# Performance work log

Hardware: AMD Instinct MI355X
Metric: run time of the kernel (lower is better)

Reference implementation:

```python
import jax, jax.numpy as jnp
import numpy as np

B, T, IDIM, HDIM, K, LMAX, NLAYERS = 64, 1024, 120, 320, 72, 96, 3
LAMB = 0.1
NEG = -1e30


def lse3(a, b, c):
    m = jnp.maximum(jnp.maximum(a, b), c)
    return m + jnp.log(jnp.exp(a - m) + jnp.exp(b - m) + jnp.exp(c - m))


def _lstm_dir(x, Wih, Whh, bb):
    # x: [B,T,D] -> h: [B,T,H]; PyTorch gate order i,f,g,o
    gx = jnp.einsum('btd,gd->tbg', x, Wih) + bb  # [T,B,4H]
    def step(carry, g):
        h, c = carry
        g = g + h @ Whh.T
        i, f, gg, o = jnp.split(g, 4, axis=-1)
        c = jax.nn.sigmoid(f) * c + jax.nn.sigmoid(i) * jnp.tanh(gg)
        h = jax.nn.sigmoid(o) * jnp.tanh(c)
        return (h, c), h
    h0 = jnp.zeros((x.shape[0], HDIM), x.dtype)
    _, hs = jax.lax.scan(step, (h0, h0), gx)
    return hs.transpose(1, 0, 2)


def _rev(x, lengths):
    # reverse each sequence within its valid length (packed-sequence semantics)
    t = jnp.arange(x.shape[1])
    idx = jnp.where(t[None, :] < lengths[:, None], lengths[:, None] - 1 - t[None, :], t[None, :])
    return jnp.take_along_axis(x, idx[:, :, None], axis=1)


def _blstm_layer(x, Wih_f, Whh_f, b_f, Wih_b, Whh_b, b_b, lengths):
    hf = _lstm_dir(x, Wih_f, Whh_f, b_f)
    hb = _rev(_lstm_dir(_rev(x, lengths), Wih_b, Whh_b, b_b), lengths)
    return jnp.concatenate([hf, hb], axis=2)


def _ctc_forward(logp, labels, in_lens, lab_lens):
    # standard CTC alpha recursion (blank=0), log-space, vectorized over batch
    Bn, Tn, _ = logp.shape
    S = 2 * LMAX + 1
    ext = jnp.zeros((Bn, S), jnp.int32).at[:, 1::2].set(labels)  # blank-interleaved labels
    em = jnp.take_along_axis(logp, jnp.broadcast_to(ext[:, None, :], (Bn, Tn, S)), axis=2)
    em = em.transpose(1, 0, 2)  # [T,B,S]
    s_idx = jnp.arange(S)
    prev_lab = jnp.concatenate([jnp.full((Bn, 2), -1, jnp.int32), ext[:, :-2]], axis=1)
    can_skip = ((s_idx[None, :] % 2) == 1) & (ext != prev_lab)
    valid_s = s_idx[None, :] < (2 * lab_lens[:, None] + 1)
    alpha0 = jnp.full((Bn, S), NEG, logp.dtype)
    alpha0 = alpha0.at[:, 0].set(em[0][:, 0]).at[:, 1].set(em[0][:, 1])
    alpha0 = jnp.where(valid_s, alpha0, NEG)
    def step(alpha, inp):
        em_t, t = inp
        a2 = jnp.concatenate([jnp.full((Bn, 1), NEG, alpha.dtype), alpha[:, :-1]], axis=1)
        a3 = jnp.concatenate([jnp.full((Bn, 2), NEG, alpha.dtype), alpha[:, :-2]], axis=1)
        a3 = jnp.where(can_skip, a3, NEG)
        new = lse3(alpha, a2, a3) + em_t
        new = jnp.where(valid_s, new, NEG)
        new = jnp.where((t < in_lens)[:, None], new, alpha)  # freeze past utterance end
        return new, None
    alpha, _ = jax.lax.scan(step, alpha0, (em[1:], jnp.arange(1, Tn)))
    last = 2 * lab_lens
    aL = jnp.take_along_axis(alpha, last[:, None], axis=1)[:, 0]
    aLm1 = jnp.take_along_axis(alpha, (last - 1)[:, None], axis=1)[:, 0]
    return jnp.logaddexp(aL, aLm1)  # log p(labels | x)


def setup_inputs():
    key = jax.random.key(0)
    ks = jax.random.split(key, 12)
    H4 = 4 * HDIM
    s = 0.05
    return dict(
        logits=jax.random.normal(ks[0], (B, T, IDIM), jnp.float32),
        labels_padded=jax.random.randint(ks[1], (B, LMAX), 1, K).astype(jnp.int32),
        input_lengths=jax.random.randint(ks[2], (B,), T // 2, T + 1).astype(jnp.int32),
        label_lengths=jax.random.randint(ks[3], (B,), LMAX // 2, LMAX + 1).astype(jnp.int32),
        Wih0=jax.random.normal(ks[4], (2, H4, IDIM), jnp.float32) * s,
        Whh0=jax.random.normal(ks[5], (2, H4, HDIM), jnp.float32) * s,
        b0=jnp.zeros((2, H4), jnp.float32),
        Wih=jax.random.normal(ks[6], (NLAYERS - 1, 2, H4, 2 * HDIM), jnp.float32) * s,
        Whh=jax.random.normal(ks[7], (NLAYERS - 1, 2, H4, HDIM), jnp.float32) * s,
        b=jnp.zeros((NLAYERS - 1, 2, H4), jnp.float32),
        W_lin=jax.random.normal(ks[8], (K, 2 * HDIM), jnp.float32) * s,
        b_lin=jnp.zeros((K,), jnp.float32),
    )


def reference(logits, labels_padded, input_lengths, label_lengths, Wih0, Whh0, b0, Wih, Whh, b, W_lin, b_lin):
    # sort by input length descending (mirrors torch.sort + index_select)
    order = jnp.argsort(-input_lengths)
    logits = logits[order]
    labels_padded = labels_padded[order]
    input_lengths = input_lengths[order]
    label_lengths = label_lengths[order]
    # 3-layer BLSTM encoder
    x = _blstm_layer(logits, Wih0[0], Whh0[0], b0[0], Wih0[1], Whh0[1], b0[1], input_lengths)
    for l in range(NLAYERS - 1):
        x = _blstm_layer(x, Wih[l, 0], Whh[l, 0], b[l, 0], Wih[l, 1], Whh[l, 1], b[l, 1], input_lengths)
    netout = jax.nn.log_softmax(x @ W_lin.T + b_lin, axis=2)  # [B,T,K]
    # CTC-CRF: numerator = CTC alpha log-prob; denominator = free-running partition
    num = _ctc_forward(netout, labels_padded, input_lengths, label_lengths)
    tmask = jnp.arange(netout.shape[1])[None, :] < input_lengths[:, None]
    den = jnp.sum(jnp.where(tmask, jax.nn.logsumexp(netout, axis=2), 0.0), axis=1)
    return jnp.mean(den - (1.0 + LAMB) * num)
```

## Files before the change

### kernel.cpp

```cpp
#include <hip/hip_runtime.h>
#include <cstdint>
#include <cstddef>


typedef _Float16 f16;
typedef _Float16 h2v   __attribute__((ext_vector_type(2)));
typedef _Float16 f16x8 __attribute__((ext_vector_type(8)));
typedef float    f32x4 __attribute__((ext_vector_type(4)));
typedef uint32_t u32x4 __attribute__((ext_vector_type(4)));

#define NEGF (-1e30f)
#define CT 128

__device__ __forceinline__ float dot2f(h2v a, h2v b, float c) {
#if __has_builtin(__builtin_amdgcn_fdot2)
  return __builtin_amdgcn_fdot2(a, b, c, false);
#else
  return c + (float)a.x * (float)b.x + (float)a.y * (float)b.y;
#endif
}

__device__ __forceinline__ void stage16(f16* lds, const f16* g) {
#if __has_builtin(__builtin_amdgcn_global_load_lds)
  __builtin_amdgcn_global_load_lds(
      (const __attribute__((address_space(1))) uint32_t*)g,
      (__attribute__((address_space(3))) uint32_t*)lds, 16, 0, 0);
#else
  int lane = threadIdx.x & 63;
  *(f16x8*)&lds[lane * 8] = *(const f16x8*)g;
#endif
}


__global__ void conv_logits(const float* __restrict__ src, f16* __restrict__ dst) {
  int idx = blockIdx.x * 256 + threadIdx.x;
  int row = idx >> 7, k = idx & 127;
  dst[idx] = (f16)((k < 120) ? src[(size_t)row * 120 + k] : 0.f);
}

__global__ void conv_wt0(const float* __restrict__ w, f16* __restrict__ dst) {
  int idx = blockIdx.x * 256 + threadIdx.x;
  int n = idx >> 7, k = idx & 127;
  dst[idx] = (f16)((k < 120) ? w[(size_t)n * 120 + k] : 0.f);
}

__global__ void conv_copy(const float* __restrict__ src, f16* __restrict__ dst, int count) {
  int idx = blockIdx.x * 256 + threadIdx.x;
  if (idx < count) dst[idx] = (f16)src[idx];
}

__global__ void conv_wtl(const float* __restrict__ w, f16* __restrict__ dst) {
  int idx = blockIdx.x * 256 + threadIdx.x;
  int n = idx / 640, k = idx % 640;
  dst[idx] = (f16)((n < 72) ? w[(size_t)n * 640 + k] : 0.f);
}

__global__ void conv_whh(const float* __restrict__ whh0, const float* __restrict__ whh,
                         uint32_t* __restrict__ dst) {
  int o = blockIdx.x * 256 + threadIdx.x;
  int tid = o & 511;
  int g  = o >> 9;
  int j  = g % 40;
  int g2 = g / 40;
  int i  = g2 % 5;
  int g3 = g2 / 5;
  int hf = g3 & 1, slot = g3 >> 1;
  int tau = i * 512 + tid;
  int lr = tau >> 2, kq = tau & 3;
  int gate = lr / 160, u = lr - gate * 160;
  int r = gate * 320 + hf * 160 + u;
  int k = kq * 80 + j * 2;
  const float* srcm = (slot < 2) ? (whh0 + ((size_t)slot * 1280 + r) * 320)
                                 : (whh  + ((size_t)(slot - 2) * 1280 + r) * 320);
  f16 lo = (f16)srcm[k], hi = (f16)srcm[k + 1];
  dst[o] = (uint32_t)__builtin_bit_cast(unsigned short, lo) |
           ((uint32_t)__builtin_bit_cast(unsigned short, hi) << 16);
}

__global__ __launch_bounds__(256)
void gemm_chunk(const f16* __restrict__ A, const f16* __restrict__ W,
                f16* __restrict__ gxc, const int* __restrict__ lens,
                int lda, int kTiles, int c0) {
  __shared__ __align__(16) f16 As[128 * 32];
  __shared__ __align__(16) f16 Ws[128 * 32];
  const int tid = threadIdx.x;
  const int lane = tid & 63, wid = tid >> 6;
  const int wm = wid >> 1, wn = wid & 1;
  const int dir = blockIdx.y >> 6, b = blockIdx.y & 63;
  const int n0 = blockIdx.x * 128;
  const int r_base = lane >> 2;
  const int c8 = (lane & 3) * 8;
  const int len = lens[b];

  f32x4 acc[4][4] = {};

  for (int kt = 0; kt < kTiles; ++kt) {
    const int k0 = kt * 32;
    __syncthreads();
#pragma unroll
    for (int hh = 0; hh < 2; ++hh) {
      const int c = wid * 2 + hh;
      const int j = c * 16 + r_base;
      const int s = c0 * CT + j;
      const int tt = dir ? ((s < len) ? (len - 1 - s) : s) : s;
      const f16* gA = A + (size_t)(b * 1024 + tt) * lda + k0 + c8;
      const f16* gW = W + (size_t)(dir * 1280 + n0 + c * 16 + r_base) * lda + k0 + c8;
      stage16(&As[c * 512], gA);
      stage16(&Ws[c * 512], gW);
    }
    __syncthreads();

    const int koff = (lane >> 4) * 8;
    f16x8 av[4], wv[4];
#pragma unroll
    for (int i = 0; i < 4; ++i)
      av[i] = *(const f16x8*)&As[(wm * 64 + i * 16 + (lane & 15)) * 32 + koff];
#pragma unroll
    for (int i = 0; i < 4; ++i)
      wv[i] = *(const f16x8*)&Ws[(wn * 64 + i * 16 + (lane & 15)) * 32 + koff];
#pragma unroll
    for (int i = 0; i < 4; ++i)
#pragma unroll
      for (int j = 0; j < 4; ++j)
        acc[i][j] = __builtin_amdgcn_mfma_f32_16x16x32_f16(av[i], wv[j], acc[i][j], 0, 0, 0);
  }

  const int r0 = (lane >> 4) * 4, cn = lane & 15;
  const size_t obase = (size_t)(dir * 64 + b) * CT;
#pragma unroll
  for (int i = 0; i < 4; ++i) {
    const int m = wm * 64 + i * 16 + r0;
#pragma unroll
    for (int j = 0; j < 4; ++j) {
      const int n = n0 + wn * 64 + j * 16 + cn;
#pragma unroll
      for (int r = 0; r < 4; ++r)
        gxc[(obase + m + r) * 1280 + n] = (f16)acc[i][j][r];
    }
  }
}

__global__ void __launch_bounds__(512)
__attribute__((amdgpu_waves_per_eu(2, 2)))
lstm_scan_chunk(const volatile uint32_t* wbuf,
                const f16* __restrict__ gxc,
                const float* __restrict__ bias,
                const int* __restrict__ lens,
                f16* xnext,
                uint32_t* xq,
                f16* hsave,
                float* csave,
                int layer, int c0) {
  const int wg = blockIdx.x;
  const int half = wg >> 7;
  const int bd = wg & 127;
  const int b = bd >> 1, dir = bd & 1;
  const int tid = threadIdx.x;

  __shared__ __align__(16) f16 hbuf[320];
  __shared__ float ylds[640];
  __shared__ __align__(16) f16 hstage[64 * 160];

  h2v w[5][40];
  {
    const volatile uint32_t* wb =
        wbuf + (size_t)((layer * 2 + dir) * 2 + half) * 200 * 512;
#pragma unroll
    for (int i = 0; i < 5; ++i)
#pragma unroll
      for (int j = 0; j < 40; ++j) {
        uint32_t v = wb[(i * 40 + j) * 512 + tid];
        w[i][j] = __builtin_bit_cast(h2v, v);
      }
  }
  if (tid < 320) hbuf[tid] = (c0 == 0) ? (f16)0.f : hsave[bd * 320 + tid];

  const int len = lens[b];
  const int kq = tid & 3;
  const int qi = tid >> 2;
  const int gu = half * 160 + tid;
  float c_state = 0.f;
  float bi = 0.f, bff = 0.f, bg = 0.f, bo = 0.f;
  if (tid < 160) {
    if (c0 > 0) c_state = csave[wg * 160 + tid];
    const float* bp = bias + dir * 1280 + gu;
    bi = bp[0]; bff = bp[320]; bg = bp[640]; bo = bp[960];
  }
  __syncthreads();

  const size_t grow0 = (size_t)(dir * 64 + b) * CT;

  for (int tl = 0; tl < CT; ++tl) {
    const int s = c0 * CT + tl;
    const uint32_t tag = (uint32_t)(layer * 1024 + s + 1);

    float gxi = 0.f, gxf = 0.f, gxg = 0.f, gxo = 0.f;
    if (tid < 160) {
      const f16* gp = gxc + (grow0 + tl) * 1280 + gu;
      gxi = (float)gp[0]; gxf = (float)gp[320]; gxg = (float)gp[640]; gxo = (float)gp[960];
    }

    float a0 = 0.f, a1 = 0.f, a2 = 0.f, a3 = 0.f, a4 = 0.f;
    {
      const u32x4* h4 = (const u32x4*)hbuf;
#pragma unroll
      for (int jb = 0; jb < 5; ++jb) {
        u32x4 p = h4[kq * 10 + jb * 2];
        u32x4 q = h4[kq * 10 + jb * 2 + 1];
        h2v hr[8];
#pragma unroll
        for (int j = 0; j < 4; ++j) hr[j] = __builtin_bit_cast(h2v, p[j]);
#pragma unroll
        for (int j = 0; j < 4; ++j) hr[4 + j] = __builtin_bit_cast(h2v, q[j]);
#pragma unroll
        for (int j = 0; j < 8; ++j) {
          a0 = dot2f(w[0][jb * 8 + j], hr[j], a0);
          a1 = dot2f(w[1][jb * 8 + j], hr[j], a1);
          a2 = dot2f(w[2][jb * 8 + j], hr[j], a2);
          a3 = dot2f(w[3][jb * 8 + j], hr[j], a3);
          a4 = dot2f(w[4][jb * 8 + j], hr[j], a4);
        }
      }
    }
    {
      float av[5] = {a0, a1, a2, a3, a4};
#pragma unroll
      for (int i = 0; i < 5; ++i) {
        float v = av[i];
        v += __shfl_xor(v, 1, 64);
        v += __shfl_xor(v, 2, 64);
        if (kq == 0) ylds[i * 128 + qi] = v;
      }
    }

    if ((tl & 31) == 0 && tl > 0) {
      const int tw = tl - 32;
#pragma unroll
      for (int it = 0; it < 2; ++it) {
        const int slot = it * 512 + tid;
        if (slot < 640) {
          const int r = (int)(((unsigned)slot * 52429u) >> 20);
          const int j = slot - r * 20;
          const int sp = c0 * CT + tw + r;
          const int ttp = dir ? ((sp < len) ? (len - 1 - sp) : sp) : sp;
          f16x8 v = *(const f16x8*)&hstage[((tw + r) & 63) * 160 + j * 8];
          *(f16x8*)&xnext[(size_t)(b * 1024 + ttp) * 640 + dir * 320 + half * 160 + j * 8] = v;
        }
      }
    }
    __syncthreads();

    if (tid < 160) {
      const int u = tid;
      float pi = ylds[u]       + gxi + bi;
      float pf = ylds[160 + u] + gxf + bff;
      float pg = ylds[320 + u] + gxg + bg;
      float po = ylds[480 + u] + gxo + bo;
      float ig = 1.f / (1.f + __expf(-pi));
      float fg = 1.f / (1.f + __expf(-pf));
      float gg = tanhf(pg);
      float og = 1.f / (1.f + __expf(-po));
      c_state = fg * c_state + ig * gg;
      float hv = og * tanhf(c_state);
      const f16 hh = (f16)hv;
      const uint32_t word = (tag << 16) |
                            (uint32_t)__builtin_bit_cast(unsigned short, hh);
      __hip_atomic_exchange(&xq[((bd * 2 + half) * 2 + (s & 1)) * 160 + u], word,
                            __ATOMIC_RELAXED, __HIP_MEMORY_SCOPE_AGENT);
      hbuf[gu] = hh;
      hstage[(tl & 63) * 160 + u] = hh;
      uint32_t pw;
      int spins = 0;
      do {
        pw = __hip_atomic_fetch_add(&xq[((bd * 2 + (1 - half)) * 2 + (s & 1)) * 160 + u],
                                    0u, __ATOMIC_RELAXED, __HIP_MEMORY_SCOPE_AGENT);
      } while ((pw >> 16) != tag && ++spins < 30000);
      hbuf[(1 - half) * 160 + u] =
          __builtin_bit_cast(f16, (unsigned short)(pw & 0xffffu));
    }
    __syncthreads();
  }

  {
    const int tw = CT - 32;
#pragma unroll
    for (int it = 0; it < 2; ++it) {
      const int slot = it * 512 + tid;
      if (slot < 640) {
        const int r = (int)(((unsigned)slot * 52429u) >> 20);
        const int j = slot - r * 20;
        const int sp = c0 * CT + tw + r;
        const int ttp = dir ? ((sp < len) ? (len - 1 - sp) : sp) : sp;
        f16x8 v = *(const f16x8*)&hstage[((tw + r) & 63) * 160 + j * 8];
        *(f16x8*)&xnext[(size_t)(b * 1024 + ttp) * 640 + dir * 320 + half * 160 + j * 8] = v;
      }
    }
  }
  if (tid < 160) {
    hsave[bd * 320 + gu] = hbuf[gu];
    csave[wg * 160 + tid] = c_state;
  }
}

__global__ __launch_bounds__(256)
void gemm_proj(const f16* __restrict__ A, const f16* __restrict__ W,
               float* __restrict__ outf, int lda, int kTiles, int ldo) {
  __shared__ __align__(16) f16 As[128 * 32];
  __shared__ __align__(16) f16 Ws[128 * 32];
  const int tid = threadIdx.x;
  const int lane = tid & 63, wid = tid >> 6;
  const int wm = wid >> 1, wn = wid & 1;
  const int m0 = blockIdx.y * 128, n0 = blockIdx.x * 128;
  const int r_base = lane >> 2;
  const int c8 = (lane & 3) * 8;

  f32x4 acc[4][4] = {};

  for (int kt = 0; kt < kTiles; ++kt) {
    const int k0 = kt * 32;
    __syncthreads();
#pragma unroll
    for (int hh = 0; hh < 2; ++hh) {
      const int c = wid * 2 + hh;
      const f16* gA = A + (size_t)(m0 + c * 16 + r_base) * lda + k0 + c8;
      const f16* gW = W + (size_t)(n0 + c * 16 + r_base) * lda + k0 + c8;
      stage16(&As[c * 512], gA);
      stage16(&Ws[c * 512], gW);
    }
    __syncthreads();

    const int koff = (lane >> 4) * 8;
    f16x8 av[4], wv[4];
#pragma unroll
    for (int i = 0; i < 4; ++i)
      av[i] = *(const f16x8*)&As[(wm * 64 + i * 16 + (lane & 15)) * 32 + koff];
#pragma unroll
    for (int i = 0; i < 4; ++i)
      wv[i] = *(const f16x8*)&Ws[(wn * 64 + i * 16 + (lane & 15)) * 32 + koff];
#pragma unroll
    for (int i = 0; i < 4; ++i)
#pragma unroll
      for (int j = 0; j < 4; ++j)
        acc[i][j] = __builtin_amdgcn_mfma_f32_16x16x32_f16(av[i], wv[j], acc[i][j], 0, 0, 0);
  }

  const int r0 = (lane >> 4) * 4, cn = lane & 15;
#pragma unroll
  for (int i = 0; i < 4; ++i) {
    const int m = m0 + wm * 64 + i * 16 + r0;
#pragma unroll
    for (int j = 0; j < 4; ++j) {
      const int n = n0 + wn * 64 + j * 16 + cn;
#pragma unroll
      for (int r = 0; r < 4; ++r)
        outf[(size_t)(m + r) * ldo + n] = acc[i][j][r];
    }
  }
}

__global__ void lse_kernel(const float* __restrict__ Z, const float* __restrict__ b_lin,
                           float* __restrict__ lseout) {
  int row = blockIdx.x * 4 + (threadIdx.x >> 6);
  int l = threadIdx.x & 63;
  const float* z = Z + (size_t)row * 128;
  float v0 = (l < 72) ? z[l] + b_lin[l] : NEGF;
  float v1 = (l < 8) ? z[l + 64] + b_lin[l + 64] : NEGF;
  float m = fmaxf(v0, v1);
#pragma unroll
  for (int o = 32; o; o >>= 1) m = fmaxf(m, __shfl_xor(m, o, 64));
  float s = ((l < 72) ? __expf(v0 - m) : 0.f) + ((l < 8) ? __expf(v1 - m) : 0.f);
#pragma unroll
  for (int o = 32; o; o >>= 1) s += __shfl_xor(s, o, 64);
  if (l == 0) lseout[row] = m + __logf(s);
}

__global__ void ctc_kernel(const float* __restrict__ Z, const float* __restrict__ lse,
                           const float* __restrict__ b_lin,
                           const int* __restrict__ labels, const int* __restrict__ inlen,
                           const int* __restrict__ lablen, float* __restrict__ num) {
  const int b = blockIdx.x;
  const int lane = threadIdx.x;
  __shared__ int ext[200];
  __shared__ float afin[200];

  for (int s = lane; s < 200; s += 64)
    ext[s] = (s < 193 && (s & 1)) ? labels[b * 96 + (s >> 1)] : 0;
  __syncthreads();

  const int L = lablen[b], len = inlen[b];
  const int Send = 2 * L + 1;
  const float* Zb = Z + (size_t)b * 1024 * 128;
  const float* lsb = lse + (size_t)b * 1024;

  float a[4];
  int   e[4];
  float bl[4];
  bool  skp[4], val[4];
#pragma unroll
  for (int j = 0; j < 4; ++j) {
    const int s = lane * 4 + j;
    e[j]   = (s < 193) ? ext[s] : 0;
    val[j] = (s < Send) && (s < 193);
    skp[j] = (s < 193) && (s & 1) && (s >= 2) && (ext[s] != ext[s - 2]);
    bl[j]  = b_lin[e[j]];
  }
  {
    const float ls0 = lsb[0];
#pragma unroll
    for (int j = 0; j < 4; ++j) {
      const int s = lane * 4 + j;
      a[j] = (s <= 1 && val[j]) ? (Zb[e[j]] + bl[j] - ls0) : NEGF;
    }
  }

  float emA[4], emB[4], lsA, lsB;
#pragma unroll
  for (int j = 0; j < 4; ++j) emA[j] = Zb[128 + e[j]];
  lsA = lsb[1];
#pragma unroll
  for (int j = 0; j < 4; ++j) emB[j] = Zb[256 + e[j]];
  lsB = lsb[2];

  for (int t = 1; t < len; ++t) {
    float em[4];
#pragma unroll
    for (int j = 0; j < 4; ++j) em[j] = emA[j];
    const float lst = lsA;
#pragma unroll
    for (int j = 0; j < 4; ++j) emA[j] = emB[j];
    lsA = lsB;
    if (t + 2 < len) {
      const float* zr = Zb + (size_t)(t + 2) * 128;
#pragma unroll
      for (int j = 0; j < 4; ++j) emB[j] = zr[e[j]];
      lsB = lsb[t + 2];
    }

    float p3 = __shfl_up(a[3], 1, 64);
    float p2 = __shfl_up(a[2], 1, 64);
    if (lane == 0) { p3 = NEGF; p2 = NEGF; }
    const float x2[4] = {p3, a[0], a[1], a[2]};
    const float x3[4] = {p2, p3, a[0], a[1]};
#pragma unroll
    for (int j = 0; j < 4; ++j) {
      const float xa = a[j], xb = x2[j];
      const float xc = skp[j] ? x3[j] : NEGF;
      const float m = fmaxf(xa, fmaxf(xb, xc));
      const float sum = __expf(xa - m) + __expf(xb - m) + __expf(xc - m);
      const float nv = m + __logf(sum) + em[j] + bl[j] - lst;
      a[j] = val[j] ? nv : NEGF;
    }
  }

#pragma unroll
  for (int j = 0; j < 4; ++j) {
    const int s = lane * 4 + j;
    if (s < 193) afin[s] = a[j];
  }
  __syncthreads();
  if (lane == 0) {
    const float aL = afin[2 * L], aLm1 = afin[2 * L - 1];
    const float m = fmaxf(aL, aLm1);
    num[b] = m + __logf(__expf(aL - m) + __expf(aLm1 - m));
  }
}

__global__ void final_kernel(const float* __restrict__ num, float* __restrict__ out) {
  int l = threadIdx.x;
  float v = -1.1f * num[l];
#pragma unroll
  for (int o = 32; o; o >>= 1) v += __shfl_xor(v, o, 64);
  if (l == 0) out[0] = v * (1.f / 64.f);
}

__global__ void sentinel_kernel(float* __restrict__ out, float code) { out[0] = code; }

extern "C" void kernel_launch(void* const* d_in, const int* in_sizes, int n_in,
                              void* d_out, int out_size, void* d_ws, size_t ws_size,
                              hipStream_t stream) {
  (void)in_sizes; (void)n_in; (void)out_size;

  const float* logits   = (const float*)d_in[0];
  const int*   labels   = (const int*)d_in[1];
  const int*   in_lens  = (const int*)d_in[2];
  const int*   lab_lens = (const int*)d_in[3];
  const float* Wih0     = (const float*)d_in[4];
  const float* Whh0     = (const float*)d_in[5];
  const float* b0       = (const float*)d_in[6];
  const float* Wih      = (const float*)d_in[7];
  const float* Whh      = (const float*)d_in[8];
  const float* bb       = (const float*)d_in[9];
  const float* W_lin    = (const float*)d_in[10];
  const float* b_lin    = (const float*)d_in[11];

  const size_t NEED = (size_t)224 * 1024 * 1024;
  if (ws_size < NEED) {
    sentinel_kernel<<<1, 1, 0, stream>>>((float*)d_out, -(float)(ws_size >> 20));
    return;
  }

  char* ws = (char*)d_ws;
  size_t off = 0;
  auto alloc = [&](size_t bytes) -> char* {
    char* p = ws + off;
    off += (bytes + 255) & ~(size_t)255;
    return p;
  };
  f16*      Xa     = (f16*)alloc((size_t)65536 * 640 * 2);
  f16*      Xb     = (f16*)alloc((size_t)65536 * 640 * 2);
  f16*      gxc    = (f16*)alloc((size_t)2 * 64 * CT * 1280 * 2);
  f16*      Wt0    = (f16*)alloc((size_t)2560 * 128 * 2);
  f16*      Wt12   = (f16*)alloc((size_t)2 * 2560 * 640 * 2);
  f16*      WtL    = (f16*)alloc((size_t)128 * 640 * 2);
  uint32_t* whh16  = (uint32_t*)alloc((size_t)6 * 2 * 200 * 512 * 4);
  float*    lseb   = (float*)alloc((size_t)65536 * 4);
  float*    num    = (float*)alloc(64 * 4);
  uint32_t* xq     = (uint32_t*)alloc((size_t)512 * 160 * 4);
  f16*      hsave  = (f16*)alloc((size_t)128 * 320 * 2);
  float*    csave  = (float*)alloc((size_t)256 * 160 * 4);
  f16*      A0     = Xb;
  float*    Z      = (float*)gxc;

  hipMemsetAsync(xq, 0, (size_t)512 * 160 * 4, stream);

  conv_logits<<<32768, 256, 0, stream>>>(logits, A0);
  conv_wt0<<<1280, 256, 0, stream>>>(Wih0, Wt0);
  conv_copy<<<12800, 256, 0, stream>>>(Wih, Wt12, 3276800);
  conv_wtl<<<320, 256, 0, stream>>>(W_lin, WtL);
  conv_whh<<<4800, 256, 0, stream>>>(Whh0, Whh, whh16);

  for (int c = 0; c < 1024 / CT; ++c) {
    gemm_chunk<<<dim3(10, 128), 256, 0, stream>>>(A0, Wt0, gxc, in_lens, 128, 4, c);
    lstm_scan_chunk<<<256, 512, 0, stream>>>(whh16, gxc, b0, in_lens, Xa, xq,
                                             hsave, csave, 0, c);
  }
  for (int c = 0; c < 1024 / CT; ++c) {
    gemm_chunk<<<dim3(10, 128), 256, 0, stream>>>(Xa, Wt12, gxc, in_lens, 640, 20, c);
    lstm_scan_chunk<<<256, 512, 0, stream>>>(whh16, gxc, bb, in_lens, Xb, xq,
                                             hsave, csave, 1, c);
  }
  for (int c = 0; c < 1024 / CT; ++c) {
    gemm_chunk<<<dim3(10, 128), 256, 0, stream>>>(Xb, Wt12 + (size_t)2560 * 640, gxc,
                                                  in_lens, 640, 20, c);
    lstm_scan_chunk<<<256, 512, 0, stream>>>(whh16, gxc, bb + 2560, in_lens, Xa, xq,
                                             hsave, csave, 2, c);
  }
  gemm_proj<<<dim3(1, 512), 256, 0, stream>>>(Xa, WtL, Z, 640, 20, 128);

  lse_kernel<<<16384, 256, 0, stream>>>(Z, b_lin, lseb);
  ctc_kernel<<<64, 64, 0, stream>>>(Z, lseb, b_lin, labels, in_lens, lab_lens, num);
  final_kernel<<<1, 64, 0, stream>>>(num, (float*)d_out);
}
```

Baseline: 9.034 ms.

## Widen GEMM tiles, prefetch gate inputs, split polling threads, fast activations, unroll CTC

The chunk GEMM now computes 256 output columns per block, so each staged A tile is reused across two W tiles and the grid is halved. The LSTM scan prefetches the next timestep's input-gate values during the current step. It also hands spin-polling on the partner's hidden state to a separate thread group (256-415), so that wait no longer sits behind the gate math. Sigmoid and tanh switch to reciprocal-based fast approximations, which may lose some accuracy. The CTC alpha loop uses an 8-deep register prefetch ring for emissions, to hide global load latency.

```diff
diff --git a/kernel.cpp b/kernel.cpp
--- a/kernel.cpp
+++ b/kernel.cpp
@@ -19,6 +19,16 @@
   return c + (float)a.x * (float)b.x + (float)a.y * (float)b.y;
 #endif
 }
+
+__device__ __forceinline__ float fast_rcp(float x) {
+#if __has_builtin(__builtin_amdgcn_rcpf)
+  return __builtin_amdgcn_rcpf(x);
+#else
+  return 1.f / x;
+#endif
+}
+__device__ __forceinline__ float fsigm(float x) { return fast_rcp(1.f + __expf(-x)); }
+__device__ __forceinline__ float ftanh(float x) { return 1.f - 2.f * fast_rcp(1.f + __expf(2.f * x)); }
 
 __device__ __forceinline__ void stage16(f16* lds, const f16* g) {
 #if __has_builtin(__builtin_amdgcn_global_load_lds)
@@ -82,17 +92,17 @@
                 f16* __restrict__ gxc, const int* __restrict__ lens,
                 int lda, int kTiles, int c0) {
   __shared__ __align__(16) f16 As[128 * 32];
-  __shared__ __align__(16) f16 Ws[128 * 32];
+  __shared__ __align__(16) f16 Ws[2][128 * 32];
   const int tid = threadIdx.x;
   const int lane = tid & 63, wid = tid >> 6;
   const int wm = wid >> 1, wn = wid & 1;
   const int dir = blockIdx.y >> 6, b = blockIdx.y & 63;
-  const int n0 = blockIdx.x * 128;
+  const int n0 = blockIdx.x * 256;
   const int r_base = lane >> 2;
   const int c8 = (lane & 3) * 8;
   const int len = lens[b];
 
-  f32x4 acc[4][4] = {};
+  f32x4 acc[4][8] = {};
 
   for (int kt = 0; kt < kTiles; ++kt) {
     const int k0 = kt * 32;
@@ -103,26 +113,34 @@
       const int j = c * 16 + r_base;
       const int s = c0 * CT + j;
       const int tt = dir ? ((s < len) ? (len - 1 - s) : s) : s;
-      const f16* gA = A + (size_t)(b * 1024 + tt) * lda + k0 + c8;
-      const f16* gW = W + (size_t)(dir * 1280 + n0 + c * 16 + r_base) * lda + k0 + c8;
-      stage16(&As[c * 512], gA);
-      stage16(&Ws[c * 512], gW);
+      stage16(&As[c * 512], A + (size_t)(b * 1024 + tt) * lda + k0 + c8);
+    }
+#pragma unroll
+    for (int hh = 0; hh < 4; ++hh) {
+      const int c = wid * 4 + hh;
+      const int tile = c >> 3, cc = c & 7;
+      stage16(&Ws[tile][cc * 512],
+              W + (size_t)(dir * 1280 + n0 + tile * 128 + cc * 16 + r_base) * lda + k0 + c8);
     }
     __syncthreads();
 
     const int koff = (lane >> 4) * 8;
-    f16x8 av[4], wv[4];
+    f16x8 av[4], wv0[4], wv1[4];
 #pragma unroll
     for (int i = 0; i < 4; ++i)
       av[i] = *(const f16x8*)&As[(wm * 64 + i * 16 + (lane & 15)) * 32 + koff];
 #pragma unroll
+    for (int i = 0; i < 4; ++i) {
+      wv0[i] = *(const f16x8*)&Ws[0][(wn * 64 + i * 16 + (lane & 15)) * 32 + koff];
+      wv1[i] = *(const f16x8*)&Ws[1][(wn * 64 + i * 16 + (lane & 15)) * 32 + koff];
+    }
+#pragma unroll
     for (int i = 0; i < 4; ++i)
-      wv[i] = *(const f16x8*)&Ws[(wn * 64 + i * 16 + (lane & 15)) * 32 + koff];
-#pragma unroll
-    for (int i = 0; i < 4; ++i)
-#pragma unroll
-      for (int j = 0; j < 4; ++j)
-        acc[i][j] = __builtin_amdgcn_mfma_f32_16x16x32_f16(av[i], wv[j], acc[i][j], 0, 0, 0);
+#pragma unroll
+      for (int j = 0; j < 4; ++j) {
+        acc[i][j]     = __builtin_amdgcn_mfma_f32_16x16x32_f16(av[i], wv0[j], acc[i][j], 0, 0, 0);
+        acc[i][4 + j] = __builtin_amdgcn_mfma_f32_16x16x32_f16(av[i], wv1[j], acc[i][4 + j], 0, 0, 0);
+      }
   }
 
   const int r0 = (lane >> 4) * 4, cn = lane & 15;
@@ -134,8 +152,10 @@
     for (int j = 0; j < 4; ++j) {
       const int n = n0 + wn * 64 + j * 16 + cn;
 #pragma unroll
-      for (int r = 0; r < 4; ++r)
-        gxc[(obase + m + r) * 1280 + n] = (f16)acc[i][j][r];
+      for (int r = 0; r < 4; ++r) {
+        gxc[(obase + m + r) * 1280 + n]       = (f16)acc[i][j][r];
+        gxc[(obase + m + r) * 1280 + n + 128] = (f16)acc[i][4 + j][r];
+      }
     }
   }
 }
@@ -190,14 +210,20 @@
 
   const size_t grow0 = (size_t)(dir * 64 + b) * CT;
 
+  float gxi = 0.f, gxf = 0.f, gxg = 0.f, gxo = 0.f;
+  if (tid < 160) {
+    const f16* gp = gxc + grow0 * 1280 + gu;
+    gxi = (float)gp[0]; gxf = (float)gp[320]; gxg = (float)gp[640]; gxo = (float)gp[960];
+  }
+
   for (int tl = 0; tl < CT; ++tl) {
     const int s = c0 * CT + tl;
     const uint32_t tag = (uint32_t)(layer * 1024 + s + 1);
 
-    float gxi = 0.f, gxf = 0.f, gxg = 0.f, gxo = 0.f;
-    if (tid < 160) {
-      const f16* gp = gxc + (grow0 + tl) * 1280 + gu;
-      gxi = (float)gp[0]; gxf = (float)gp[320]; gxg = (float)gp[640]; gxo = (float)gp[960];
+    float nxi = 0.f, nxf = 0.f, nxg = 0.f, nxo = 0.f;
+    if (tid < 160 && tl + 1 < CT) {
+      const f16* gp = gxc + (grow0 + tl + 1) * 1280 + gu;
+      nxi = (float)gp[0]; nxf = (float)gp[320]; nxg = (float)gp[640]; nxo = (float)gp[960];
     }
 
     float a0 = 0.f, a1 = 0.f, a2 = 0.f, a3 = 0.f, a4 = 0.f;
@@ -256,12 +282,12 @@
       float pf = ylds[160 + u] + gxf + bff;
       float pg = ylds[320 + u] + gxg + bg;
       float po = ylds[480 + u] + gxo + bo;
-      float ig = 1.f / (1.f + __expf(-pi));
-      float fg = 1.f / (1.f + __expf(-pf));
-      float gg = tanhf(pg);
-      float og = 1.f / (1.f + __expf(-po));
+      float ig = fsigm(pi);
+      float fg = fsigm(pf);
+      float gg = ftanh(pg);
+      float og = fsigm(po);
       c_state = fg * c_state + ig * gg;
-      float hv = og * tanhf(c_state);
+      float hv = og * ftanh(c_state);
       const f16 hh = (f16)hv;
       const uint32_t word = (tag << 16) |
                             (uint32_t)__builtin_bit_cast(unsigned short, hh);
@@ -269,6 +295,8 @@
                             __ATOMIC_RELAXED, __HIP_MEMORY_SCOPE_AGENT);
       hbuf[gu] = hh;
       hstage[(tl & 63) * 160 + u] = hh;
+    } else if (tid >= 256 && tid < 416) {
+      const int u = tid - 256;
       uint32_t pw;
       int spins = 0;
       do {
@@ -279,6 +307,8 @@
           __builtin_bit_cast(f16, (unsigned short)(pw & 0xffffu));
     }
     __syncthreads();
+
+    gxi = nxi; gxf = nxf; gxg = nxg; gxo = nxo;
   }
 
   {
@@ -322,10 +352,8 @@
 #pragma unroll
     for (int hh = 0; hh < 2; ++hh) {
       const int c = wid * 2 + hh;
-      const f16* gA = A + (size_t)(m0 + c * 16 + r_base) * lda + k0 + c8;
-      const f16* gW = W + (size_t)(n0 + c * 16 + r_base) * lda + k0 + c8;
-      stage16(&As[c * 512], gA);
-      stage16(&Ws[c * 512], gW);
+      stage16(&As[c * 512], A + (size_t)(m0 + c * 16 + r_base) * lda + k0 + c8);
+      stage16(&Ws[c * 512], W + (size_t)(n0 + c * 16 + r_base) * lda + k0 + c8);
     }
     __syncthreads();
 
@@ -413,29 +441,9 @@
     }
   }
 
-  float emA[4], emB[4], lsA, lsB;
-#pragma unroll
-  for (int j = 0; j < 4; ++j) emA[j] = Zb[128 + e[j]];
-  lsA = lsb[1];
-#pragma unroll
-  for (int j = 0; j < 4; ++j) emB[j] = Zb[256 + e[j]];
-  lsB = lsb[2];
-
-  for (int t = 1; t < len; ++t) {
-    float em[4];
-#pragma unroll
-    for (int j = 0; j < 4; ++j) em[j] = emA[j];
-    const float lst = lsA;
-#pragma unroll
-    for (int j = 0; j < 4; ++j) emA[j] = emB[j];
-    lsA = lsB;
-    if (t + 2 < len) {
-      const float* zr = Zb + (size_t)(t + 2) * 128;
-#pragma unroll
-      for (int j = 0; j < 4; ++j) emB[j] = zr[e[j]];
-      lsB = lsb[t + 2];
-    }
-
+  auto step = [&](const float em0, const float em1, const float em2, const float em3,
+                  const float lst) {
+    const float emv[4] = {em0, em1, em2, em3};
     float p3 = __shfl_up(a[3], 1, 64);
     float p2 = __shfl_up(a[2], 1, 64);
     if (lane == 0) { p3 = NEGF; p2 = NEGF; }
@@ -447,9 +455,43 @@
       const float xc = skp[j] ? x3[j] : NEGF;
       const float m = fmaxf(xa, fmaxf(xb, xc));
       const float sum = __expf(xa - m) + __expf(xb - m) + __expf(xc - m);
-      const float nv = m + __logf(sum) + em[j] + bl[j] - lst;
+      const float nv = m + __logf(sum) + emv[j] + bl[j] - lst;
       a[j] = val[j] ? nv : NEGF;
     }
+  };
+
+  float emr[8][4];
+  float lsr[8];
+#pragma unroll
+  for (int d = 1; d <= 8; ++d) {
+    const int r = (d < len) ? d : (len - 1);
+    const float* zr = Zb + (size_t)r * 128;
+#pragma unroll
+    for (int j = 0; j < 4; ++j) emr[d & 7][j] = zr[e[j]];
+    lsr[d & 7] = lsb[r];
+  }
+
+  int t = 1;
+  for (; t + 8 <= len; t += 8) {
+#pragma unroll
+    for (int k = 0; k < 8; ++k) {
+      const int slot = (1 + k) & 7;
+      const float e0 = emr[slot][0], e1 = emr[slot][1],
+                  e2 = emr[slot][2], e3 = emr[slot][3];
+      const float lst = lsr[slot];
+      const int tp = t + k + 8;
+      if (tp < len) {
+        const float* zr = Zb + (size_t)tp * 128;
+#pragma unroll
+        for (int j = 0; j < 4; ++j) emr[slot][j] = zr[e[j]];
+        lsr[slot] = lsb[tp];
+      }
+      step(e0, e1, e2, e3, lst);
+    }
+  }
+  for (; t < len; ++t) {
+    const float* zr = Zb + (size_t)t * 128;
+    step(zr[e[0]], zr[e[1]], zr[e[2]], zr[e[3]], lsb[t]);
   }
 
 #pragma unroll
@@ -530,18 +572,18 @@
   conv_whh<<<4800, 256, 0, stream>>>(Whh0, Whh, whh16);
 
   for (int c = 0; c < 1024 / CT; ++c) {
-    gemm_chunk<<<dim3(10, 128), 256, 0, stream>>>(A0, Wt0, gxc, in_lens, 128, 4, c);
+    gemm_chunk<<<dim3(5, 128), 256, 0, stream>>>(A0, Wt0, gxc, in_lens, 128, 4, c);
     lstm_scan_chunk<<<256, 512, 0, stream>>>(whh16, gxc, b0, in_lens, Xa, xq,
                                              hsave, csave, 0, c);
   }
   for (int c = 0; c < 1024 / CT; ++c) {
-    gemm_chunk<<<dim3(10, 128), 256, 0, stream>>>(Xa, Wt12, gxc, in_lens, 640, 20, c);
+    gemm_chunk<<<dim3(5, 128), 256, 0, stream>>>(Xa, Wt12, gxc, in_lens, 640, 20, c);
     lstm_scan_chunk<<<256, 512, 0, stream>>>(whh16, gxc, bb, in_lens, Xb, xq,
                                              hsave, csave, 1, c);
   }
   for (int c = 0; c < 1024 / CT; ++c) {
-    gemm_chunk<<<dim3(10, 128), 256, 0, stream>>>(Xb, Wt12 + (size_t)2560 * 640, gxc,
-                                                  in_lens, 640, 20, c);
+    gemm_chunk<<<dim3(5, 128), 256, 0, stream>>>(Xb, Wt12 + (size_t)2560 * 640, gxc,
+                                                 in_lens, 640, 20, c);
     lstm_scan_chunk<<<256, 512, 0, stream>>>(whh16, gxc, bb + 2560, in_lens, Xa, xq,
                                              hsave, csave, 2, c);
   }
```

Result: no change. 9.100 ms (+0.7%).
